# Performance work log

Measured on AMD Instinct MI355X. Metric: run time of the kernel, lower is better.

Reference implementation:

```python
import jax, jax.numpy as jnp
import numpy as np

B, L, E, H = 4, 2048, 1024, 16
D = E // H
RBF_GAMMA = 0.5


def setup_inputs() -> dict:
    key = jax.random.key(0)
    ks = jax.random.split(key, 8)
    s = 1.0 / np.sqrt(E)  # linear init scale
    return {
        "query": jax.random.normal(ks[0], (B, L, E), jnp.float32),
        "key": jax.random.normal(ks[1], (B, L, E), jnp.float32),
        "value": jax.random.normal(ks[2], (B, L, E), jnp.float32),
        "Wq": jax.random.normal(ks[3], (E, E), jnp.float32) * s,
        "bq": jnp.zeros((E,), jnp.float32),
        "Wk": jax.random.normal(ks[4], (E, E), jnp.float32) * s,
        "bk": jnp.zeros((E,), jnp.float32),
        "Wv": jax.random.normal(ks[5], (E, E), jnp.float32) * s,
        "bv": jnp.zeros((E,), jnp.float32),
        "Wo": jax.random.normal(ks[6], (E, E), jnp.float32) * s,
        "bo": jnp.zeros((E,), jnp.float32),
    }


def _heads(x):
    # (B, L, E) -> (B, H, L, D)
    b, l, _ = x.shape
    return x.reshape(b, l, H, D).transpose(0, 2, 1, 3)


def _rbf_scores(q, k):
    # score[b,h,i,j] = -gamma * ||q_i - k_j||^2   (log of RBF kernel)
    q2 = jnp.sum(q * q, axis=-1)  # (B,H,Lq)
    k2 = jnp.sum(k * k, axis=-1)  # (B,H,Lk)
    qk = jnp.einsum("bhqd,bhkd->bhqk", q, k)  # (B,H,Lq,Lk)
    sqd = q2[..., :, None] + k2[..., None, :] - 2.0 * qk
    return -RBF_GAMMA * sqd


def reference(query, key, value, Wq, bq, Wk, bk, Wv, bv, Wo, bo):
    # Linear projections (torch nn.Linear: x @ W.T + b)
    q = _heads(query @ Wq.T + bq)
    k = _heads(key @ Wk.T + bk)
    v = _heads(value @ Wv.T + bv)
    scores = _rbf_scores(q, k)            # (B,H,L,L)
    attn = jax.nn.softmax(scores, axis=-1)  # dropout p=0.0 (eval)
    out = jnp.einsum("bhqk,bhkd->bhqd", attn, v)
    out = out.transpose(0, 2, 1, 3).reshape(B, L, E)  # merge heads
    return out @ Wo.T + bo
```

## Files before the change

### kernel.cpp

```cpp
#include <hip/hip_runtime.h>
#include <hip/hip_bf16.h>
#include <stdint.h>

#define DEV __device__ __forceinline__

typedef __attribute__((ext_vector_type(8))) __bf16 bf16x8;
typedef __attribute__((ext_vector_type(4))) float f32x4;
typedef __attribute__((ext_vector_type(16))) float f32x16;
typedef __attribute__((ext_vector_type(4))) unsigned int u32x4;

#define LOG2E 1.44269504088896f

DEV unsigned short f2bf(float f) {
    union { float f; unsigned int u; } v; v.f = f;
    unsigned int u = v.u;
    return (unsigned short)((u + 0x7FFFu + ((u >> 16) & 1u)) >> 16);
}
DEV float bf2f(unsigned short s) {
    union { unsigned int u; float f; } v; v.u = ((unsigned int)s) << 16;
    return v.f;
}

DEV f32x4 mfma16(bf16x8 a, bf16x8 b, f32x4 c) {
    return __builtin_amdgcn_mfma_f32_16x16x32_bf16(a, b, c, 0, 0, 0);
}
DEV f32x16 mfma32(bf16x8 a, bf16x8 b, f32x16 c) {
    return __builtin_amdgcn_mfma_f32_32x32x16_bf16(a, b, c, 0, 0, 0);
}
DEV float exp2a(float x) { float r; asm("v_exp_f32 %0, %1" : "=v"(r) : "v"(x)); return r; }
DEV unsigned cvtpk(float lo, float hi) {
    unsigned r; asm("v_cvt_pk_bf16_f32 %0, %1, %2" : "=v"(r) : "v"(lo), "v"(hi)); return r;
}
DEV void plswap(unsigned& x, unsigned& y) {
    asm volatile("v_permlane32_swap_b32 %0, %1" : "+v"(x), "+v"(y));
}

#define GLOAD_LDS16(g, l)                                                          \
    __builtin_amdgcn_global_load_lds((__attribute__((address_space(1))) void*)(g), \
                                     (__attribute__((address_space(3))) void*)(l), \
                                     16, 0, 0)

__global__ void k_cvtw(const float* __restrict__ i0, const float* __restrict__ i1,
                       const float* __restrict__ i2, const float* __restrict__ i3,
                       unsigned short* __restrict__ o0, unsigned short* __restrict__ o1,
                       unsigned short* __restrict__ o2, unsigned short* __restrict__ o3) {
    int z = blockIdx.y;
    const float* in = z == 0 ? i0 : (z == 1 ? i1 : (z == 2 ? i2 : i3));
    unsigned short* out = z == 0 ? o0 : (z == 1 ? o1 : (z == 2 ? o2 : o3));
    float scale = z == 0 ? LOG2E : 1.0f;
    int stride = gridDim.x * blockDim.x;
    for (int i = blockIdx.x * blockDim.x + threadIdx.x; i * 4 < 1048576; i += stride) {
        float4 f = reinterpret_cast<const float4*>(in)[i];
        ushort4 o;
        o.x = f2bf(f.x * scale); o.y = f2bf(f.y * scale);
        o.z = f2bf(f.z * scale); o.w = f2bf(f.w * scale);
        reinterpret_cast<ushort4*>(out)[i] = o;
    }
}

__global__ __launch_bounds__(256) void k_gemm_qkv(
    const float* __restrict__ aq, const float* __restrict__ ak, const float* __restrict__ av,
    const unsigned short* __restrict__ wq, const unsigned short* __restrict__ wk,
    const unsigned short* __restrict__ wv,
    const float* __restrict__ bq, const float* __restrict__ bk, const float* __restrict__ bv,
    unsigned short* __restrict__ Qb, unsigned short* __restrict__ Kb,
    unsigned short* __restrict__ Vb, float* __restrict__ biask) {
    __shared__ __align__(16) unsigned short As[128 * 64];
    __shared__ __align__(16) unsigned short Bs[128 * 64];
    const int flat = blockIdx.x;
    const int xcd = flat & 7;
    const int bn = (flat >> 3) & 7;
    const int row = xcd * 24 + (flat >> 6);
    const int z = row >> 6;
    const int bm = row & 63;

    const float* A = z == 0 ? aq : (z == 1 ? ak : av);
    const unsigned short* Bw = z == 0 ? wq : (z == 1 ? wk : wv);
    const float* bias = z == 0 ? bq : (z == 1 ? bk : bv);
    const float bscale = z == 0 ? LOG2E : 1.0f;
    const int K = 1024;

    const int tid = threadIdx.x;
    const int lane = tid & 63, w = tid >> 6;
    const int g = lane >> 4, cc = lane & 15;
    const int wm = w >> 1, wn = w & 1;

    f32x4 acc[4][4] = {};
    const int srow = lane >> 3;
    const int scol = (lane & 7) * 8;

    float4 ar[4][2];
    auto loadA = [&](int kt) {
#pragma unroll
        for (int p = 0; p < 4; ++p) {
            int c = w * 4 + p;
            int rr = c * 8 + srow;
            const float* gA = A + (size_t)(bm * 128 + rr) * K + kt + scol;
            ar[p][0] = *reinterpret_cast<const float4*>(gA);
            ar[p][1] = *reinterpret_cast<const float4*>(gA + 4);
        }
    };
    auto writeA = [&]() {
#pragma unroll
        for (int p = 0; p < 4; ++p) {
            int c = w * 4 + p;
            u32x4 pk;
            pk[0] = cvtpk(ar[p][0].x, ar[p][0].y);
            pk[1] = cvtpk(ar[p][0].z, ar[p][0].w);
            pk[2] = cvtpk(ar[p][1].x, ar[p][1].y);
            pk[3] = cvtpk(ar[p][1].z, ar[p][1].w);
            *reinterpret_cast<u32x4*>(&As[c * 512 + srow * 64 + scol]) = pk;
        }
    };

    loadA(0);
    for (int kt = 0; kt < K; kt += 64) {
        writeA();
        if (kt + 64 < K) loadA(kt + 64);
#pragma unroll
        for (int p = 0; p < 4; ++p) {
            int c = w * 4 + p;
            int rr = c * 8 + srow;
            const unsigned short* gB = Bw + (size_t)(bn * 128 + rr) * K + kt + scol;
            GLOAD_LDS16(gB, &Bs[c * 512]);
        }
        __syncthreads();
#pragma unroll
        for (int kc = 0; kc < 2; ++kc) {
            bf16x8 af[4], bf[4];
#pragma unroll
            for (int i = 0; i < 4; ++i) {
                af[i] = *reinterpret_cast<const bf16x8*>(&As[(wm * 64 + i * 16 + cc) * 64 + kc * 32 + g * 8]);
                bf[i] = *reinterpret_cast<const bf16x8*>(&Bs[(wn * 64 + i * 16 + cc) * 64 + kc * 32 + g * 8]);
            }
#pragma unroll
            for (int mi = 0; mi < 4; ++mi)
#pragma unroll
                for (int nj = 0; nj < 4; ++nj)
                    acc[mi][nj] = mfma16(af[mi], bf[nj], acc[mi][nj]);
        }
        __syncthreads();
    }

    unsigned short* out = z == 0 ? Qb : (z == 1 ? Kb : Vb);
    float sq[4][4];
#pragma unroll
    for (int mi = 0; mi < 4; ++mi)
#pragma unroll
        for (int r = 0; r < 4; ++r) sq[mi][r] = 0.f;

#pragma unroll
    for (int mi = 0; mi < 4; ++mi) {
#pragma unroll
        for (int nj = 0; nj < 4; ++nj) {
            int n = bn * 128 + wn * 64 + nj * 16 + cc;
            float bvv = bias[n] * bscale;
            int h = n >> 6, d = n & 63;
#pragma unroll
            for (int r = 0; r < 4; ++r) {
                int m = bm * 128 + wm * 64 + mi * 16 + g * 4 + r;
                unsigned short us = f2bf(acc[mi][nj][r] + bvv);
                int b = m >> 11, l = m & 2047;
                out[(((size_t)b * 16 + h) * 2048 + l) * 64 + d] = us;
                if (z == 1) { float vr = bf2f(us); sq[mi][r] += vr * vr; }
            }
        }
    }
    if (z == 1) {
        const int h = bn * 2 + wn;
#pragma unroll
        for (int mi = 0; mi < 4; ++mi)
#pragma unroll
            for (int r = 0; r < 4; ++r) {
                float s = sq[mi][r];
                s += __shfl_xor(s, 1); s += __shfl_xor(s, 2);
                s += __shfl_xor(s, 4); s += __shfl_xor(s, 8);
                if (cc == 0) {
                    int m = bm * 128 + wm * 64 + mi * 16 + g * 4 + r;
                    biask[(((size_t)(m >> 11)) * 16 + h) * 2048 + (m & 2047)] =
                        -0.5f * LOG2E * s;
                }
            }
    }
}

__global__ __launch_bounds__(256) void k_vt(const unsigned short* __restrict__ Vb,
                                            unsigned short* __restrict__ VbT) {
    __shared__ __align__(16) unsigned short T[64 * 72];
    const int blk = blockIdx.x;
    const int bh = blk >> 5, lt = blk & 31;
    const int tid = threadIdx.x;
    const int rr = tid >> 3, seg = tid & 7;
#pragma unroll
    for (int p = 0; p < 2; ++p) {
        int row = p * 32 + rr;
        const unsigned short* src = Vb + ((size_t)bh * 2048 + lt * 64 + row) * 64 + seg * 8;
        *reinterpret_cast<u32x4*>(&T[row * 72 + seg * 8]) = *reinterpret_cast<const u32x4*>(src);
    }
    __syncthreads();
#pragma unroll
    for (int p = 0; p < 2; ++p) {
        int d = p * 32 + rr;
        union { u32x4 v; unsigned short s[8]; } o;
#pragma unroll
        for (int j = 0; j < 8; ++j) o.s[j] = T[(seg * 8 + j) * 72 + d];
        unsigned short* dst = VbT + ((size_t)bh * 64 + d) * 2048 + lt * 64 + seg * 8;
        *reinterpret_cast<u32x4*>(dst) = o.v;
    }
}

__global__ __launch_bounds__(256) void k_gemm_out(const unsigned short* __restrict__ A,
                                                  const unsigned short* __restrict__ Bw,
                                                  const float* __restrict__ bias,
                                                  float* __restrict__ out) {
    __shared__ __align__(16) unsigned short As[128 * 64];
    __shared__ __align__(16) unsigned short Bs[128 * 64];
    const int K = 1024, N = 1024;
    const int flat = blockIdx.x;
    const int xcd = flat & 7;
    const int bn = (flat >> 3) & 7;
    const int bm = xcd * 8 + (flat >> 6);

    const int tid = threadIdx.x;
    const int lane = tid & 63, w = tid >> 6;
    const int g = lane >> 4, cc = lane & 15;
    const int wm = w >> 1, wn = w & 1;

    f32x4 acc[4][4] = {};
    const int srow = lane >> 3;
    const int scol = (lane & 7) * 8;

    for (int kt = 0; kt < K; kt += 64) {
#pragma unroll
        for (int p = 0; p < 4; ++p) {
            int c = w * 4 + p;
            int rr = c * 8 + srow;
            const unsigned short* gA = A + (size_t)(bm * 128 + rr) * K + kt + scol;
            GLOAD_LDS16(gA, &As[c * 512]);
            const unsigned short* gB = Bw + (size_t)(bn * 128 + rr) * K + kt + scol;
            GLOAD_LDS16(gB, &Bs[c * 512]);
        }
        __syncthreads();
#pragma unroll
        for (int kc = 0; kc < 2; ++kc) {
            bf16x8 af[4], bf[4];
#pragma unroll
            for (int i = 0; i < 4; ++i) {
                af[i] = *reinterpret_cast<const bf16x8*>(&As[(wm * 64 + i * 16 + cc) * 64 + kc * 32 + g * 8]);
                bf[i] = *reinterpret_cast<const bf16x8*>(&Bs[(wn * 64 + i * 16 + cc) * 64 + kc * 32 + g * 8]);
            }
#pragma unroll
            for (int mi = 0; mi < 4; ++mi)
#pragma unroll
                for (int nj = 0; nj < 4; ++nj)
                    acc[mi][nj] = mfma16(af[mi], bf[nj], acc[mi][nj]);
        }
        __syncthreads();
    }

#pragma unroll
    for (int mi = 0; mi < 4; ++mi) {
#pragma unroll
        for (int nj = 0; nj < 4; ++nj) {
            int n = bn * 128 + wn * 64 + nj * 16 + cc;
            float bvv = bias[n];
#pragma unroll
            for (int r = 0; r < 4; ++r) {
                int m = bm * 128 + wm * 64 + mi * 16 + g * 4 + r;
                out[(size_t)m * N + n] = acc[mi][nj][r] + bvv;
            }
        }
    }
}

__global__ __launch_bounds__(256, 2) void k_attn5(const unsigned short* __restrict__ Q,
                                                  const unsigned short* __restrict__ K,
                                                  const unsigned short* __restrict__ VT,
                                                  const float* __restrict__ biask,
                                                  unsigned short* __restrict__ Ob) {
    __shared__ __align__(16) unsigned short SM[18432];
    const int tid = threadIdx.x;
    const int lane = tid & 63, w = tid >> 6;
    const int l31 = lane & 31, hi = lane >> 5, l7 = lane & 7;
    const int flat = blockIdx.x;
    const int bh = (flat & 7) * 8 + ((flat >> 3) & 7);
    const int qt = flat >> 6;
    const size_t kvbase = (size_t)bh * 2048 * 64;
    const int q0 = qt * 256 + w * 64;

    bf16x8 qf[2][4];
#pragma unroll
    for (int qb = 0; qb < 2; ++qb)
#pragma unroll
        for (int kc = 0; kc < 4; ++kc)
            qf[qb][kc] = *reinterpret_cast<const bf16x8*>(
                Q + kvbase + (size_t)(q0 + qb * 32 + l31) * 64 + kc * 16 + hi * 8);

    f32x16 ot[2][2] = {};
    float lrun[2] = {0.f, 0.f};
    const int srow = lane >> 3;

    auto stage = [&](int buf, int t) {
        const int kO = buf ? 4096 : 0;
        const int vO = buf ? 12288 : 8192;
#pragma unroll
        for (int i = 0; i < 2; ++i) {
            int r = w * 16 + i * 8 + srow;
            int cb = l7 ^ (r & 7);
            const unsigned short* gk = K + kvbase + (size_t)(t * 64 + r) * 64 + cb * 8;
            GLOAD_LDS16(gk, &SM[kO + (w * 16 + i * 8) * 64]);
            const unsigned short* gv = VT + kvbase + (size_t)r * 2048 + t * 64 + cb * 8;
            GLOAD_LDS16(gv, &SM[vO + (w * 16 + i * 8) * 64]);
        }
        if (w == 0 && lane < 16) {
            const float* gb = biask + bh * 2048 + t * 64 + lane * 4;
            GLOAD_LDS16(gb, &SM[buf ? 16512 : 16384]);
        }
    };

    stage(0, 0);
    int cur = 0;
    for (int t = 0; t < 32; ++t) {
        __syncthreads();
        if (t + 1 < 32) stage(cur ^ 1, t + 1);
        const int kO = cur ? 4096 : 0;
        const int vO = cur ? 12288 : 8192;
        const float* Bl = reinterpret_cast<const float*>(&SM[cur ? 16512 : 16384]);

        f32x4 bb[2][4];
#pragma unroll
        for (int t2 = 0; t2 < 2; ++t2)
#pragma unroll
            for (int g2 = 0; g2 < 4; ++g2)
                bb[t2][g2] = *reinterpret_cast<const f32x4*>(Bl + t2 * 32 + g2 * 8 + hi * 4);

        f32x16 st[2][2];
#pragma unroll
        for (int qb = 0; qb < 2; ++qb)
#pragma unroll
            for (int t2 = 0; t2 < 2; ++t2)
#pragma unroll
                for (int g2 = 0; g2 < 4; ++g2)
#pragma unroll
                    for (int j = 0; j < 4; ++j) st[qb][t2][g2 * 4 + j] = bb[t2][g2][j];

        __builtin_amdgcn_s_setprio(1);
#pragma unroll
        for (int kc = 0; kc < 4; ++kc)
#pragma unroll
            for (int t2 = 0; t2 < 2; ++t2) {
                bf16x8 kf = *reinterpret_cast<const bf16x8*>(
                    &SM[kO + (t2 * 32 + l31) * 64 + ((((kc << 1) | hi) ^ l7) << 3)]);
                st[0][t2] = mfma32(kf, qf[0][kc], st[0][t2]);
                st[1][t2] = mfma32(kf, qf[1][kc], st[1][t2]);
            }
        __builtin_amdgcn_s_setprio(0);

#pragma unroll
        for (int qb = 0; qb < 2; ++qb) {
            float r0 = 0.f, r1 = 0.f;
#pragma unroll
            for (int i = 0; i < 16; ++i) {
                float p0 = exp2a(st[qb][0][i]); st[qb][0][i] = p0; r0 += p0;
                float p1 = exp2a(st[qb][1][i]); st[qb][1][i] = p1; r1 += p1;
            }
            lrun[qb] += r0 + r1;
        }

#pragma unroll
        for (int t2 = 0; t2 < 2; ++t2) {
            bf16x8 fA[2], fB[2];
#pragma unroll
            for (int qb = 0; qb < 2; ++qb) {
                unsigned w0 = cvtpk(st[qb][t2][0], st[qb][t2][1]);
                unsigned w1 = cvtpk(st[qb][t2][2], st[qb][t2][3]);
                unsigned w2 = cvtpk(st[qb][t2][4], st[qb][t2][5]);
                unsigned w3 = cvtpk(st[qb][t2][6], st[qb][t2][7]);
                unsigned w4 = cvtpk(st[qb][t2][8], st[qb][t2][9]);
                unsigned w5 = cvtpk(st[qb][t2][10], st[qb][t2][11]);
                unsigned w6 = cvtpk(st[qb][t2][12], st[qb][t2][13]);
                unsigned w7 = cvtpk(st[qb][t2][14], st[qb][t2][15]);
                plswap(w0, w2); plswap(w1, w3); plswap(w4, w6); plswap(w5, w7);
                u32x4 p0, p1;
                p0[0] = w0; p0[1] = w1; p0[2] = w2; p0[3] = w3;
                p1[0] = w4; p1[1] = w5; p1[2] = w6; p1[3] = w7;
                fA[qb] = __builtin_bit_cast(bf16x8, p0);
                fB[qb] = __builtin_bit_cast(bf16x8, p1);
            }
            const int kb0 = t2 * 2, kb1 = t2 * 2 + 1;
            __builtin_amdgcn_s_setprio(1);
#pragma unroll
            for (int dj = 0; dj < 2; ++dj) {
                bf16x8 v0 = *reinterpret_cast<const bf16x8*>(
                    &SM[vO + (dj * 32 + l31) * 64 + ((((kb0 << 1) | hi) ^ l7) << 3)]);
                bf16x8 v1 = *reinterpret_cast<const bf16x8*>(
                    &SM[vO + (dj * 32 + l31) * 64 + ((((kb1 << 1) | hi) ^ l7) << 3)]);
                ot[0][dj] = mfma32(v0, fA[0], ot[0][dj]);
                ot[0][dj] = mfma32(v1, fB[0], ot[0][dj]);
                ot[1][dj] = mfma32(v0, fA[1], ot[1][dj]);
                ot[1][dj] = mfma32(v1, fB[1], ot[1][dj]);
            }
            __builtin_amdgcn_s_setprio(0);
        }
        cur ^= 1;
    }

    lrun[0] += __shfl_xor(lrun[0], 32);
    lrun[1] += __shfl_xor(lrun[1], 32);

    __syncthreads();
#pragma unroll
    for (int qb = 0; qb < 2; ++qb) {
        float inv = 1.0f / lrun[qb];
        const int base = (w * 64 + qb * 32 + l31) * 72;
#pragma unroll
        for (int dj = 0; dj < 2; ++dj)
#pragma unroll
            for (int i = 0; i < 8; ++i) {
                unsigned pr = cvtpk(ot[qb][dj][2 * i] * inv, ot[qb][dj][2 * i + 1] * inv);
                int d0 = dj * 32 + 2 * (i & 1) + 8 * (i >> 1) + 4 * hi;
                *reinterpret_cast<unsigned*>(&SM[base + d0]) = pr;
            }
    }
    __syncthreads();
    const int b = bh >> 4, h = bh & 15;
#pragma unroll
    for (int pass = 0; pass < 8; ++pass) {
        int row = pass * 32 + (tid >> 3);
        int seg = tid & 7;
        u32x4 vdat = *reinterpret_cast<const u32x4*>(&SM[row * 72 + seg * 8]);
        int l = qt * 256 + row;
        *reinterpret_cast<u32x4*>(Ob + ((size_t)b * 2048 + l) * 1024 + h * 64 + seg * 8) = vdat;
    }
}

extern "C" void kernel_launch(void* const* d_in, const int* in_sizes, int n_in,
                              void* d_out, int out_size, void* d_ws, size_t ws_size,
                              hipStream_t stream) {
    const float* query = (const float*)d_in[0];
    const float* key   = (const float*)d_in[1];
    const float* value = (const float*)d_in[2];
    const float* Wq = (const float*)d_in[3];
    const float* bq = (const float*)d_in[4];
    const float* Wk = (const float*)d_in[5];
    const float* bk = (const float*)d_in[6];
    const float* Wv = (const float*)d_in[7];
    const float* bv = (const float*)d_in[8];
    const float* Wo = (const float*)d_in[9];
    const float* bo = (const float*)d_in[10];

    unsigned short* VbT = (unsigned short*)d_ws;
    unsigned short* wq = VbT + 8388608;
    unsigned short* wk = wq + 1048576;
    unsigned short* wv = wk + 1048576;
    unsigned short* wo = wv + 1048576;
    unsigned short* Qb = wo + 1048576;
    unsigned short* Kb = Qb + 8388608;
    unsigned short* Vb = Kb + 8388608;
    unsigned short* Ob = Vb + 8388608;
    float* biask = (float*)(Ob + 8388608);

    k_cvtw<<<dim3(256, 4), 256, 0, stream>>>(Wq, Wk, Wv, Wo, wq, wk, wv, wo);

    k_gemm_qkv<<<1536, 256, 0, stream>>>(query, key, value, wq, wk, wv,
                                         bq, bk, bv, Qb, Kb, Vb, biask);

    k_vt<<<2048, 256, 0, stream>>>(Vb, VbT);

    k_attn5<<<512, 256, 0, stream>>>(Qb, Kb, VbT, biask, Ob);

    k_gemm_out<<<512, 256, 0, stream>>>(Ob, wo, bo, (float*)d_out);
}
```

Before: 213.9 us.

## Double-buffer B tiles in QKV GEMM and fuse V transpose into epilogue

The QKV projection GEMM now double-buffers the weight tile in LDS and controls the pipeline with explicit vmcnt/lgkmcnt waits and raw barriers, so the next weight load overlaps the current MFMA work. The V-projection blocks now transpose their output tile through LDS and write V directly in the (b,h,d,l) layout, which removes the separate k_vt kernel and its extra pass over V in global memory. LDS use grows to 48 KB per block, which can lower occupancy, and the hand-counted waitcnt values must stay in step with the number of loads issued.

```diff
diff --git a/kernel.cpp b/kernel.cpp
--- a/kernel.cpp
+++ b/kernel.cpp
@@ -7,6 +7,7 @@
 typedef __attribute__((ext_vector_type(8))) __bf16 bf16x8;
 typedef __attribute__((ext_vector_type(4))) float f32x4;
 typedef __attribute__((ext_vector_type(16))) float f32x16;
+typedef __attribute__((ext_vector_type(2))) unsigned int u32x2;
 typedef __attribute__((ext_vector_type(4))) unsigned int u32x4;
 
 #define LOG2E 1.44269504088896f
@@ -39,6 +40,10 @@
     __builtin_amdgcn_global_load_lds((__attribute__((address_space(1))) void*)(g), \
                                      (__attribute__((address_space(3))) void*)(l), \
                                      16, 0, 0)
+
+#define VMCNT(N) asm volatile("s_waitcnt vmcnt(" #N ")" ::: "memory")
+#define LGKM0    asm volatile("s_waitcnt lgkmcnt(0)" ::: "memory")
+#define RBAR()   do { __builtin_amdgcn_s_barrier(); __builtin_amdgcn_sched_barrier(0); } while (0)
 
 __global__ void k_cvtw(const float* __restrict__ i0, const float* __restrict__ i1,
                        const float* __restrict__ i2, const float* __restrict__ i3,
@@ -64,9 +69,11 @@
     const unsigned short* __restrict__ wv,
     const float* __restrict__ bq, const float* __restrict__ bk, const float* __restrict__ bv,
     unsigned short* __restrict__ Qb, unsigned short* __restrict__ Kb,
-    unsigned short* __restrict__ Vb, float* __restrict__ biask) {
-    __shared__ __align__(16) unsigned short As[128 * 64];
-    __shared__ __align__(16) unsigned short Bs[128 * 64];
+    unsigned short* __restrict__ VbT, float* __restrict__ biask) {
+    __shared__ __align__(16) unsigned short SMEM[24576];
+    unsigned short* As = SMEM;
+    unsigned short* Bs = SMEM + 8192;
+
     const int flat = blockIdx.x;
     const int xcd = flat & 7;
     const int bn = (flat >> 3) & 7;
@@ -112,26 +119,24 @@
             *reinterpret_cast<u32x4*>(&As[c * 512 + srow * 64 + scol]) = pk;
         }
     };
-
-    loadA(0);
-    for (int kt = 0; kt < K; kt += 64) {
-        writeA();
-        if (kt + 64 < K) loadA(kt + 64);
+    auto issueB = [&](int kt, int buf) {
 #pragma unroll
         for (int p = 0; p < 4; ++p) {
             int c = w * 4 + p;
             int rr = c * 8 + srow;
             const unsigned short* gB = Bw + (size_t)(bn * 128 + rr) * K + kt + scol;
-            GLOAD_LDS16(gB, &Bs[c * 512]);
-        }
-        __syncthreads();
+            GLOAD_LDS16(gB, &Bs[buf * 8192 + c * 512]);
+        }
+    };
+    auto compute = [&](int buf) {
+        const unsigned short* Bc = &Bs[buf * 8192];
 #pragma unroll
         for (int kc = 0; kc < 2; ++kc) {
             bf16x8 af[4], bf[4];
 #pragma unroll
             for (int i = 0; i < 4; ++i) {
                 af[i] = *reinterpret_cast<const bf16x8*>(&As[(wm * 64 + i * 16 + cc) * 64 + kc * 32 + g * 8]);
-                bf[i] = *reinterpret_cast<const bf16x8*>(&Bs[(wn * 64 + i * 16 + cc) * 64 + kc * 32 + g * 8]);
+                bf[i] = *reinterpret_cast<const bf16x8*>(&Bc[(wn * 64 + i * 16 + cc) * 64 + kc * 32 + g * 8]);
             }
 #pragma unroll
             for (int mi = 0; mi < 4; ++mi)
@@ -139,10 +144,66 @@
                 for (int nj = 0; nj < 4; ++nj)
                     acc[mi][nj] = mfma16(af[mi], bf[nj], acc[mi][nj]);
         }
+    };
+
+    loadA(0);
+    issueB(0, 0);
+    issueB(64, 1);
+    VMCNT(8);
+    writeA();
+    loadA(64);
+    VMCNT(12);
+    LGKM0; RBAR();
+    compute(0);
+    RBAR();
+    for (int kt = 64; kt < 960; kt += 64) {
+        int c = (kt >> 6) & 1;
+        issueB(kt + 64, c ^ 1);
+        VMCNT(4);
+        writeA();
+        loadA(kt + 64);
+        LGKM0; RBAR();
+        compute(c);
+        RBAR();
+    }
+    VMCNT(0);
+    writeA();
+    LGKM0; RBAR();
+    compute(1);
+
+    if (z == 2) {
         __syncthreads();
-    }
-
-    unsigned short* out = z == 0 ? Qb : (z == 1 ? Kb : Vb);
+        unsigned short* T = SMEM;
+#pragma unroll
+        for (int mi = 0; mi < 4; ++mi) {
+#pragma unroll
+            for (int nj = 0; nj < 4; ++nj) {
+                int nl = wn * 64 + nj * 16 + cc;
+                float bvv = bias[bn * 128 + nl];
+                int m0 = wm * 64 + mi * 16 + g * 4;
+                u32x2 pr;
+                pr[0] = cvtpk(acc[mi][nj][0] + bvv, acc[mi][nj][1] + bvv);
+                pr[1] = cvtpk(acc[mi][nj][2] + bvv, acc[mi][nj][3] + bvv);
+                *reinterpret_cast<u32x2*>(&T[nl * 136 + m0]) = pr;
+            }
+        }
+        __syncthreads();
+        const int b = bm >> 4;
+        const int l0 = (bm & 15) * 128;
+        const int h0 = bn * 2;
+#pragma unroll
+        for (int p = 0; p < 8; ++p) {
+            int n = p * 16 + (tid >> 4);
+            int chunk = tid & 15;
+            u32x4 v = *reinterpret_cast<const u32x4*>(&T[n * 136 + chunk * 8]);
+            int h = h0 + (n >> 6), d = n & 63;
+            *reinterpret_cast<u32x4*>(
+                &VbT[(((size_t)b * 16 + h) * 64 + d) * 2048 + l0 + chunk * 8]) = v;
+        }
+        return;
+    }
+
+    unsigned short* out = z == 0 ? Qb : Kb;
     float sq[4][4];
 #pragma unroll
     for (int mi = 0; mi < 4; ++mi)
@@ -181,31 +242,6 @@
                         -0.5f * LOG2E * s;
                 }
             }
-    }
-}
-
-__global__ __launch_bounds__(256) void k_vt(const unsigned short* __restrict__ Vb,
-                                            unsigned short* __restrict__ VbT) {
-    __shared__ __align__(16) unsigned short T[64 * 72];
-    const int blk = blockIdx.x;
-    const int bh = blk >> 5, lt = blk & 31;
-    const int tid = threadIdx.x;
-    const int rr = tid >> 3, seg = tid & 7;
-#pragma unroll
-    for (int p = 0; p < 2; ++p) {
-        int row = p * 32 + rr;
-        const unsigned short* src = Vb + ((size_t)bh * 2048 + lt * 64 + row) * 64 + seg * 8;
-        *reinterpret_cast<u32x4*>(&T[row * 72 + seg * 8]) = *reinterpret_cast<const u32x4*>(src);
-    }
-    __syncthreads();
-#pragma unroll
-    for (int p = 0; p < 2; ++p) {
-        int d = p * 32 + rr;
-        union { u32x4 v; unsigned short s[8]; } o;
-#pragma unroll
-        for (int j = 0; j < 8; ++j) o.s[j] = T[(seg * 8 + j) * 72 + d];
-        unsigned short* dst = VbT + ((size_t)bh * 64 + d) * 2048 + lt * 64 + seg * 8;
-        *reinterpret_cast<u32x4*>(dst) = o.v;
     }
 }
 
@@ -456,16 +492,13 @@
     unsigned short* wo = wv + 1048576;
     unsigned short* Qb = wo + 1048576;
     unsigned short* Kb = Qb + 8388608;
-    unsigned short* Vb = Kb + 8388608;
-    unsigned short* Ob = Vb + 8388608;
+    unsigned short* Ob = Kb + 8388608;
     float* biask = (float*)(Ob + 8388608);
 
     k_cvtw<<<dim3(256, 4), 256, 0, stream>>>(Wq, Wk, Wv, Wo, wq, wk, wv, wo);
 
     k_gemm_qkv<<<1536, 256, 0, stream>>>(query, key, value, wq, wk, wv,
-                                         bq, bk, bv, Qb, Kb, Vb, biask);
-
-    k_vt<<<2048, 256, 0, stream>>>(Vb, VbT);
+                                         bq, bk, bv, Qb, Kb, VbT, biask);
 
     k_attn5<<<512, 256, 0, stream>>>(Qb, Kb, VbT, biask, Ob);
 
```

Result: faster. 198.0 us (-7.4%).
